# Optimization experiments

Hardware: AMD Instinct MI355X
Metric: run time of the kernel (lower is better)

## Reference

```python
import jax, jax.numpy as jnp
import numpy as np
from jax import lax

B, UD, YD, ZD, H, L, T = 256, 16, 16, 32, 128, 2, 2048


def _lin_params(key, out_dim, in_dim):
    k1, k2 = jax.random.split(key)
    s = 1.0 / np.sqrt(in_dim)
    w = jax.random.uniform(k1, (out_dim, in_dim), minval=-s, maxval=s, dtype=jnp.float32)
    b = jax.random.uniform(k2, (out_dim,), minval=-s, maxval=s, dtype=jnp.float32)
    return w, b


def setup_inputs() -> dict:
    key = jax.random.key(0)
    ks = iter(jax.random.split(key, 24))
    d = {}
    d["u"] = jax.random.normal(next(ks), (B, UD, T), dtype=jnp.float32)
    d["y"] = jax.random.normal(next(ks), (B, YD, T), dtype=jnp.float32)
    d["h0"] = jax.random.uniform(next(ks), (L, B, H), dtype=jnp.float32)  # torch.rand init
    d["phi_u_w1"], d["phi_u_b1"] = _lin_params(next(ks), H, UD)
    d["phi_u_w2"], d["phi_u_b2"] = _lin_params(next(ks), H, H)
    d["dynn_w1"], d["dynn_b1"] = _lin_params(next(ks), H, 2 * H)
    d["dynn_w2"], d["dynn_b2"] = _lin_params(next(ks), H, H)
    d["x_mean_w"], d["x_mean_b"] = _lin_params(next(ks), ZD, H)
    d["phi_x_w1"], d["phi_x_b1"] = _lin_params(next(ks), H, ZD)
    d["phi_x_w2"], d["phi_x_b2"] = _lin_params(next(ks), H, H)
    d["menn_w1"], d["menn_b1"] = _lin_params(next(ks), H, H)
    d["menn_w2"], d["menn_b2"] = _lin_params(next(ks), YD, H)
    s = 1.0 / np.sqrt(H)
    d["gru_wih"] = jax.random.uniform(next(ks), (L, 3 * H, H), minval=-s, maxval=s, dtype=jnp.float32)
    d["gru_whh"] = jax.random.uniform(next(ks), (L, 3 * H, H), minval=-s, maxval=s, dtype=jnp.float32)
    return d


def _mlp(x, w1, b1, w2, b2):
    # Linear -> ReLU -> Linear (torch Linear convention: x @ W.T + b)
    return jax.nn.relu(x @ w1.T + b1) @ w2.T + b2


def _gru_step(h, x_in, wih, whh):
    # h: (L, B, H); x_in: (B, H); nn.GRU with bias=False
    new_h = []
    inp = x_in
    for l in range(L):
        gi = inp @ wih[l].T           # (B, 3H)
        gh = h[l] @ whh[l].T          # (B, 3H)
        i_r, i_z, i_n = jnp.split(gi, 3, axis=-1)
        h_r, h_z, h_n = jnp.split(gh, 3, axis=-1)
        r = jax.nn.sigmoid(i_r + h_r)
        z = jax.nn.sigmoid(i_z + h_z)
        n = jnp.tanh(i_n + r * h_n)
        hl = (1.0 - z) * n + z * h[l]
        new_h.append(hl)
        inp = hl
    return jnp.stack(new_h)


def reference(u, y, h0, phi_u_w1, phi_u_b1, phi_u_w2, phi_u_b2,
              dynn_w1, dynn_b1, dynn_w2, dynn_b2, x_mean_w, x_mean_b,
              phi_x_w1, phi_x_b1, phi_x_w2, phi_x_b2,
              menn_w1, menn_b1, menn_w2, menn_b2, gru_wih, gru_whh):
    # mpnt_wt = -1 branch (0 >= mpnt_wt > -10): pure NN dynamics + measurement
    u_t = jnp.transpose(u, (2, 0, 1))  # (T, B, UD)
    y_t = jnp.transpose(y, (2, 0, 1))  # (T, B, YD)
    # phi_u has no recurrent dependency -> precompute over all timesteps
    pu = _mlp(u_t, phi_u_w1, phi_u_b1, phi_u_w2, phi_u_b2)  # (T, B, H)

    def step(h, inputs):
        pu_t, yt = inputs
        d = _mlp(jnp.concatenate([pu_t, h[-1]], axis=1), dynn_w1, dynn_b1, dynn_w2, dynn_b2)
        x_t = d @ x_mean_w.T + x_mean_b                 # (B, ZD)
        h_new = _gru_step(h, pu_t, gru_wih, gru_whh)
        px = _mlp(x_t, phi_x_w1, phi_x_b1, phi_x_w2, phi_x_b2)
        y_hat = _mlp(px, menn_w1, menn_b1, menn_w2, menn_b2)
        loss_t = jnp.sum((y_hat - yt) ** 2)
        return h_new, loss_t

    _, losses = lax.scan(step, h0, (pu, y_t))
    return jnp.sum(losses)
```

## Files before the change

### kernel.cpp

```cpp
#include <hip/hip_runtime.h>
#include <hip/hip_bf16.h>

#define TT 2048
#define BB 256
#define HH 128
#define UDIM 16
#define YDIM 16
#define ZDIM 32
#define H3 384

typedef __hip_bfloat16 bf16;
typedef _Float16 half2v __attribute__((ext_vector_type(2)));

constexpr int clog2(int x) { return x <= 1 ? 0 : 1 + clog2(x >> 1); }

template <int M_, int K_, int O_, bool RELU_>
__device__ __forceinline__ void rstage(const float* __restrict__ wfrag,
                                       const float* __restrict__ xin, int XS,
                                       float* __restrict__ ps,
                                       const float* __restrict__ bias,
                                       float* __restrict__ outb)
{
    constexpr int F = K_ / O_;
    const int T = threadIdx.x;
    const int jb = T & (M_ / 2 - 1);
    const int o  = T >> clog2(M_ / 2);
#pragma unroll
    for (int r = 0; r < 8; ++r) {
        float a0 = 0.f, a1 = 0.f;
#pragma unroll
        for (int g = 0; g < F; g += 4) {
            const float4 xv = *reinterpret_cast<const float4*>(&xin[r * XS + o * F + g]);
            a0 += xv.x * wfrag[g]     + xv.y * wfrag[g + 1]
                + xv.z * wfrag[g + 2] + xv.w * wfrag[g + 3];
            a1 += xv.x * wfrag[F + g]     + xv.y * wfrag[F + g + 1]
                + xv.z * wfrag[F + g + 2] + xv.w * wfrag[F + g + 3];
        }
        ps[r * 1024 + o * M_ + jb]           = a0;
        ps[r * 1024 + o * M_ + jb + M_ / 2]  = a1;
    }
    __syncthreads();
    for (int oi = T; oi < 8 * M_; oi += 512) {
        const int r = oi >> clog2(M_);
        const int j = oi & (M_ - 1);
        float s = bias[j];
#pragma unroll
        for (int o2 = 0; o2 < O_; ++o2) s += ps[r * 1024 + o2 * M_ + j];
        if (RELU_) s = fmaxf(s, 0.f);
        outb[r * M_ + j] = s;
    }
    __syncthreads();
}

template <int M_, int K_, int O_>
__device__ __forceinline__ void loadw(float* __restrict__ wfrag, const float* __restrict__ Wg)
{
    constexpr int F = K_ / O_;
    const int T = threadIdx.x;
    const int jb = T & (M_ / 2 - 1);
    const int o  = T >> clog2(M_ / 2);
#pragma unroll
    for (int h = 0; h < 2; ++h)
#pragma unroll
        for (int g = 0; g < F; g += 4)
            *reinterpret_cast<float4*>(&wfrag[h * F + g]) =
                *reinterpret_cast<const float4*>(&Wg[(jb + h * (M_ / 2)) * K_ + o * F + g]);
}

template <int M_, int K_, int O_>
__device__ __forceinline__ void loadw_h(half2v* __restrict__ wfrag, const float* __restrict__ Wg)
{
    constexpr int F = K_ / O_;
    const int T = threadIdx.x;
    const int jb = T & (M_ / 2 - 1);
    const int o  = T >> clog2(M_ / 2);
#pragma unroll
    for (int h = 0; h < 2; ++h)
#pragma unroll
        for (int g = 0; g < F / 2; ++g) {
            const float* s = &Wg[(jb + h * (M_ / 2)) * K_ + o * F + 2 * g];
            half2v v; v.x = (_Float16)s[0]; v.y = (_Float16)s[1];
            wfrag[h * (F / 2) + g] = v;
        }
}

template <int M_, int K_, int O_, bool RELU_>
__device__ __forceinline__ void rstage_h(const half2v* __restrict__ wfrag,
                                         const _Float16* __restrict__ xin, int XS,
                                         float* __restrict__ ps,
                                         const float* __restrict__ bias,
                                         _Float16* __restrict__ outb)
{
    constexpr int F = K_ / O_;
    constexpr int FH = F / 2;
    const int T = threadIdx.x;
    const int jb = T & (M_ / 2 - 1);
    const int o  = T >> clog2(M_ / 2);
#pragma unroll
    for (int r = 0; r < 8; ++r) {
        float a0 = 0.f, a1 = 0.f;
        const half2v* xv = reinterpret_cast<const half2v*>(xin + r * XS + o * F);
        if constexpr (FH >= 4) {
#pragma unroll
            for (int g4 = 0; g4 < FH / 4; ++g4) {
                half2v xt[4];
                *reinterpret_cast<float4*>(xt) = reinterpret_cast<const float4*>(xv)[g4];
#pragma unroll
                for (int e = 0; e < 4; ++e) {
                    a0 = __builtin_amdgcn_fdot2(xt[e], wfrag[g4 * 4 + e], a0, false);
                    a1 = __builtin_amdgcn_fdot2(xt[e], wfrag[FH + g4 * 4 + e], a1, false);
                }
            }
        } else {
            half2v xt[2];
            *reinterpret_cast<float2*>(xt) = *reinterpret_cast<const float2*>(xv);
            a0 = __builtin_amdgcn_fdot2(xt[0], wfrag[0], a0, false);
            a0 = __builtin_amdgcn_fdot2(xt[1], wfrag[1], a0, false);
            a1 = __builtin_amdgcn_fdot2(xt[0], wfrag[FH], a1, false);
            a1 = __builtin_amdgcn_fdot2(xt[1], wfrag[FH + 1], a1, false);
        }
        ps[r * 1024 + o * M_ + jb]           = a0;
        ps[r * 1024 + o * M_ + jb + M_ / 2]  = a1;
    }
    __syncthreads();
    for (int oi = T; oi < 8 * M_; oi += 512) {
        const int r = oi >> clog2(M_);
        const int j = oi & (M_ - 1);
        float s = bias[j];
#pragma unroll
        for (int o2 = 0; o2 < O_; ++o2) s += ps[r * 1024 + o2 * M_ + j];
        if (RELU_) s = fmaxf(s, 0.f);
        outb[r * M_ + j] = (_Float16)s;
    }
    __syncthreads();
}

__global__ __launch_bounds__(512, 2) void phi_u_kernel(
    const float* __restrict__ u, const float* __restrict__ w1, const float* __restrict__ b1,
    const float* __restrict__ w2, const float* __restrict__ b2,
    bf16* __restrict__ pu, int s0, int nrows)
{
    __shared__ __align__(16) float ps[8192];
    __shared__ __align__(16) float xc[8 * 16];
    __shared__ __align__(16) float bP[8 * 128];
    __shared__ __align__(16) float bias_l[256];
    const int T = threadIdx.x;
    if (T < 128) { bias_l[T] = b1[T]; bias_l[128 + T] = b2[T]; }
    const int jb = T & 63, o = T >> 6;
    float wa[4];
    wa[0] = w1[jb * 16 + o * 2];        wa[1] = w1[jb * 16 + o * 2 + 1];
    wa[2] = w1[(jb + 64) * 16 + o * 2]; wa[3] = w1[(jb + 64) * 16 + o * 2 + 1];
    float wb[32]; loadw<128, 128, 8>(wb, w2);
    __syncthreads();

    for (int tile = blockIdx.x; tile < nrows / 32; tile += gridDim.x) {
        const int n0 = tile * 32;
        const int b  = s0 + (n0 >> 11);
        const int t0 = n0 & (TT - 1);
#pragma unroll 1
        for (int rb = 0; rb < 4; ++rb) {
            if (T < 128) {
                const int r = T & 7, c = T >> 3;
                xc[r * 16 + c] = u[((size_t)b * UDIM + c) * TT + t0 + rb * 8 + r];
            }
            __syncthreads();
#pragma unroll
            for (int r = 0; r < 8; ++r) {
                const float x0 = xc[r * 16 + o * 2], x1 = xc[r * 16 + o * 2 + 1];
                ps[r * 1024 + o * 128 + jb]      = x0 * wa[0] + x1 * wa[1];
                ps[r * 1024 + o * 128 + jb + 64] = x0 * wa[2] + x1 * wa[3];
            }
            __syncthreads();
            for (int oi = T; oi < 8 * 128; oi += 512) {
                const int r = oi >> 7, j = oi & 127;
                float s = bias_l[j];
#pragma unroll
                for (int o2 = 0; o2 < 8; ++o2) s += ps[r * 1024 + o2 * 128 + j];
                bP[r * 128 + j] = fmaxf(s, 0.f);
            }
            __syncthreads();
            rstage<128, 128, 8, false>(wb, bP, 128, ps, bias_l + 128, bP);
            const int row0 = n0 + rb * 8;
            for (int oi = T; oi < 8 * 128; oi += 512) {
                const int r = oi >> 7, j = oi & 127;
                pu[(size_t)(row0 + r) * HH + j] = __float2bfloat16(bP[r * 128 + j]);
            }
            __syncthreads();
        }
    }
}

__device__ __forceinline__ void gmv(const half2v w[6][16], const _Float16* __restrict__ vb,
                                    int o, float* __restrict__ psL, int psb)
{
    const half2v* vec2 = reinterpret_cast<const half2v*>(vb) + o * 16;
    float a0 = 0.f, a1 = 0.f, a2 = 0.f, a3 = 0.f, a4 = 0.f, a5 = 0.f;
#pragma unroll
    for (int k4 = 0; k4 < 4; ++k4) {
        half2v xt[4];
        *reinterpret_cast<float4*>(xt) = reinterpret_cast<const float4*>(vec2)[k4];
#pragma unroll
        for (int e = 0; e < 4; ++e) {
            const int k = k4 * 4 + e;
            a0 = __builtin_amdgcn_fdot2(xt[e], w[0][k], a0, false);
            a1 = __builtin_amdgcn_fdot2(xt[e], w[1][k], a1, false);
            a2 = __builtin_amdgcn_fdot2(xt[e], w[2][k], a2, false);
            a3 = __builtin_amdgcn_fdot2(xt[e], w[3][k], a3, false);
            a4 = __builtin_amdgcn_fdot2(xt[e], w[4][k], a4, false);
            a5 = __builtin_amdgcn_fdot2(xt[e], w[5][k], a5, false);
        }
    }
    psL[psb]       = a0; psL[psb + 64]  = a1; psL[psb + 128] = a2;
    psL[psb + 192] = a3; psL[psb + 256] = a4; psL[psb + 320] = a5;
}

__global__ __launch_bounds__(512, 2) void gru_fused_kernel(
    const bf16* __restrict__ pu_in,
    const float* __restrict__ wih,
    const float* __restrict__ whh,
    const float* __restrict__ h0_g,
    bf16* __restrict__ hlast,
    int s0)
{
    const int t = threadIdx.x;
    __shared__ __align__(16) _Float16 x0h[HH];
    __shared__ __align__(16) _Float16 x1h[2][HH];
    __shared__ __align__(16) _Float16 h0h[HH];
    __shared__ __align__(16) _Float16 h1h[HH];
    __shared__ __align__(16) float ps[2 * 3072];

    const int g = t >> 6;
    const int m = g >> 2, o = g & 3;
    const int u = t & 63;
    const float* WbaseA = ((m == 0) ? wih : whh);
    const float* WbaseB = WbaseA + (size_t)H3 * HH;
    half2v wA[6][16], wB[6][16];
#pragma unroll
    for (int i = 0; i < 6; ++i) {
        const float* sA = &WbaseA[(u + 64 * i) * HH + o * 32];
        const float* sB = &WbaseB[(u + 64 * i) * HH + o * 32];
#pragma unroll
        for (int k = 0; k < 16; ++k) {
            half2v v; v.x = (_Float16)sA[2 * k]; v.y = (_Float16)sA[2 * k + 1];
            wA[i][k] = v;
            half2v w2; w2.x = (_Float16)sB[2 * k]; w2.y = (_Float16)sB[2 * k + 1];
            wB[i][k] = w2;
        }
    }
    float* psA = ps;
    float* psB = ps + 3072;
    const int psb = o * 768 + m * 384 + u;

    const bf16* xb = pu_in + (size_t)blockIdx.x * TT * HH;
    bf16* ob = hlast + (size_t)blockIdx.x * TT * HH;

    float hreg = 0.f;
    if (t < HH) {
        hreg = h0_g[(size_t)(s0 + blockIdx.x) * HH + t];
        h0h[t] = (_Float16)hreg;
        x0h[t] = (_Float16)__bfloat162float(xb[t]);
    } else if (t < 2 * HH) {
        const int j = t - HH;
        hreg = h0_g[((size_t)BB + s0 + blockIdx.x) * HH + j];
        h1h[j] = (_Float16)hreg;
    }
    __syncthreads();

#pragma unroll 1
    for (int i = 0; i <= TT; ++i) {
        float xnext = 0.f;
        if (t < HH && i + 1 < TT)
            xnext = __bfloat162float(xb[(size_t)(i + 1) * HH + t]);
        if (i < TT)  gmv(wA, (m == 0) ? x0h : h0h, o, psA, psb);
        if (i >= 1)  gmv(wB, (m == 0) ? x1h[(i + 1) & 1] : h1h, o, psB, psb);
        __syncthreads();
        if (t < HH) {
            if (i < TT) {
                const int j = t;
                float gir = 0.f, giz = 0.f, gin = 0.f, ghr = 0.f, ghz = 0.f, ghn = 0.f;
#pragma unroll
                for (int o2 = 0; o2 < 4; ++o2) {
                    const float* pp = psA + o2 * 768;
                    gir += pp[j];        giz += pp[128 + j]; gin += pp[256 + j];
                    ghr += pp[384 + j];  ghz += pp[512 + j]; ghn += pp[640 + j];
                }
                const float rg = 1.f / (1.f + __expf(-(gir + ghr)));
                const float zg = 1.f / (1.f + __expf(-(giz + ghz)));
                const float narg = gin + rg * ghn;
                const float e2 = __expf(2.f * fabsf(narg));
                float ng = 1.f - 2.f / (e2 + 1.f);
                ng = (narg < 0.f) ? -ng : ng;
                const float hn = (1.f - zg) * ng + zg * hreg;
                h0h[j] = (_Float16)hn;
                x1h[i & 1][j] = (_Float16)hn;
                x0h[j] = (_Float16)xnext;
                hreg = hn;
            }
        } else if (t < 2 * HH) {
            if (i >= 1) {
                const int j = t - HH;
                float gir = 0.f, giz = 0.f, gin = 0.f, ghr = 0.f, ghz = 0.f, ghn = 0.f;
#pragma unroll
                for (int o2 = 0; o2 < 4; ++o2) {
                    const float* pp = psB + o2 * 768;
                    gir += pp[j];        giz += pp[128 + j]; gin += pp[256 + j];
                    ghr += pp[384 + j];  ghz += pp[512 + j]; ghn += pp[640 + j];
                }
                const float rg = 1.f / (1.f + __expf(-(gir + ghr)));
                const float zg = 1.f / (1.f + __expf(-(giz + ghz)));
                const float narg = gin + rg * ghn;
                const float e2 = __expf(2.f * fabsf(narg));
                float ng = 1.f - 2.f / (e2 + 1.f);
                ng = (narg < 0.f) ? -ng : ng;
                ob[(size_t)(i - 1) * HH + j] = __float2bfloat16(hreg);
                const float hn = (1.f - zg) * ng + zg * hreg;
                h1h[j] = (_Float16)hn;
                hreg = hn;
            }
        }
        __syncthreads();
    }
}

__device__ __forceinline__ void stage_xc_h(_Float16* __restrict__ xc,
                                           const bf16* __restrict__ pu,
                                           const bf16* __restrict__ hl,
                                           int n0, int rb)
{
    const int T = threadIdx.x;
    const int base = n0 + rb * 8;
#pragma unroll
    for (int i = 0; i < 4; ++i) {
        const int idx = T + i * 512;
        const int r = idx >> 8, k = idx & 255;
        const size_t row = (size_t)(base + r);
        xc[r * 256 + k] = (_Float16)((k < 128) ? __bfloat162float(pu[row * HH + k])
                                               : __bfloat162float(hl[row * HH + (k - 128)]));
    }
}

__global__ __launch_bounds__(512, 4) void head_kernel(
    const bf16* __restrict__ pu, const bf16* __restrict__ hlast, const float* __restrict__ y_g,
    const float* __restrict__ dw1, const float* __restrict__ db1,
    const float* __restrict__ dw2, const float* __restrict__ db2,
    const float* __restrict__ xw, const float* __restrict__ xb,
    const float* __restrict__ pxw1, const float* __restrict__ pxb1,
    const float* __restrict__ pxw2, const float* __restrict__ pxb2,
    const float* __restrict__ mw1, const float* __restrict__ mb1,
    const float* __restrict__ mw2, const float* __restrict__ mb2,
    float* __restrict__ out, int s0, int nrows)
{
    __shared__ __align__(16) float ps[8192];
    __shared__ __align__(16) _Float16 xc[8 * 256];
    __shared__ __align__(16) _Float16 bP[8 * 128];
    __shared__ __align__(16) _Float16 bQ[8 * 128];
    __shared__ __align__(16) float bias_l[528];
    __shared__ float red[8];
    const int T = threadIdx.x;

    if (T < 128) bias_l[T]       = db1[T];
    if (T < 128) bias_l[256 + T] = pxb2[T];
    if (T < 128) bias_l[384 + T] = mb1[T];
    if (T < 16)  bias_l[512 + T] = mb2[T];

    for (int idx = T; idx < 4096; idx += 512) {
        const int z = idx >> 7, k = idx & 127;
        float s = 0.f;
        for (int m2 = 0; m2 < 128; ++m2) s += xw[z * 128 + m2] * dw2[m2 * 128 + k];
        ps[idx] = s;
    }
    if (T < 32) {
        float c = xb[T];
        for (int m2 = 0; m2 < 128; ++m2) c += xw[T * 128 + m2] * db2[m2];
        ps[4096 + T] = c;
    }
    __syncthreads();
    half2v wc[16];
    {
        const int jbw = T & 63, ow = T >> 6;
#pragma unroll
        for (int h = 0; h < 2; ++h) {
            const int j = jbw + h * 64;
#pragma unroll
            for (int gg = 0; gg < 8; ++gg) {
                const int k0 = ow * 16 + 2 * gg;
                float s0 = 0.f, s1 = 0.f;
#pragma unroll
                for (int z = 0; z < 32; ++z) {
                    const float p = pxw1[j * 32 + z];
                    s0 += p * ps[z * 128 + k0];
                    s1 += p * ps[z * 128 + k0 + 1];
                }
                half2v v; v.x = (_Float16)s0; v.y = (_Float16)s1;
                wc[h * 8 + gg] = v;
            }
        }
    }
    if (T < 128) {
        float s = pxb1[T];
#pragma unroll
        for (int z = 0; z < 32; ++z) s += pxw1[T * 32 + z] * ps[4096 + z];
        bias_l[128 + T] = s;
    }

    half2v w1[32]; loadw_h<128, 256, 8 >(w1, dw1);
    half2v w5[16]; loadw_h<128, 128, 8 >(w5, pxw2);
    half2v w6[16]; loadw_h<128, 128, 8 >(w6, mw1);
    const int jb7 = T & 7, o7 = T >> 3;
    half2v w7a, w7b;
    w7a.x = (_Float16)mw2[jb7 * 128 + 2 * o7];
    w7a.y = (_Float16)mw2[jb7 * 128 + 2 * o7 + 1];
    w7b.x = (_Float16)mw2[(jb7 + 8) * 128 + 2 * o7];
    w7b.y = (_Float16)mw2[(jb7 + 8) * 128 + 2 * o7 + 1];

    float lossreg = 0.f;

    for (int tile = blockIdx.x; tile < nrows / 32; tile += gridDim.x) {
        const int n0 = tile * 32;
        const int b  = s0 + (n0 >> 11);
        const int t0 = n0 & (TT - 1);
        stage_xc_h(xc, pu, hlast, n0, 0);
#pragma unroll 1
        for (int rb = 0; rb < 4; ++rb) {
            __syncthreads();
            rstage_h<128, 256, 8, true >(w1, xc, 256, ps, bias_l + 0,   bP);
            rstage_h<128, 128, 8, true >(wc, bP, 128, ps, bias_l + 128, bQ);
            rstage_h<128, 128, 8, false>(w5, bQ, 128, ps, bias_l + 256, bP);
            rstage_h<128, 128, 8, true >(w6, bP, 128, ps, bias_l + 384, bQ);
#pragma unroll
            for (int r = 0; r < 8; ++r) {
                const half2v xv = *reinterpret_cast<const half2v*>(&bQ[r * 128 + 2 * o7]);
                ps[r * 1024 + o7 * 16 + jb7]     = __builtin_amdgcn_fdot2(xv, w7a, 0.f, false);
                ps[r * 1024 + o7 * 16 + jb7 + 8] = __builtin_amdgcn_fdot2(xv, w7b, 0.f, false);
            }
            if (rb < 3) stage_xc_h(xc, pu, hlast, n0, rb + 1);
            __syncthreads();
            if (T < 128) {
                const int r = T >> 4, j = T & 15;
                float s = bias_l[512 + j];
#pragma unroll
                for (int o2 = 0; o2 < 64; ++o2) s += ps[r * 1024 + o2 * 16 + j];
                const int trow = t0 + rb * 8 + r;
                const float yv = y_g[((size_t)b * YDIM + j) * TT + trow];
                const float d = s - yv;
                lossreg += d * d;
            }
        }
    }
    __syncthreads();
#pragma unroll
    for (int off = 32; off > 0; off >>= 1) lossreg += __shfl_down(lossreg, off, 64);
    if ((T & 63) == 0) red[T >> 6] = lossreg;
    __syncthreads();
    if (T == 0) {
        float s = 0.f;
#pragma unroll
        for (int i = 0; i < 8; ++i) s += red[i];
        atomicAdd(out, s);
    }
}

__global__ void zero_out_kernel(float* o) { o[0] = 0.f; }

extern "C" void kernel_launch(void* const* d_in, const int* in_sizes, int n_in,
                              void* d_out, int out_size, void* d_ws, size_t ws_size,
                              hipStream_t stream)
{
    (void)in_sizes; (void)n_in; (void)out_size;
    const float* u    = (const float*)d_in[0];
    const float* y    = (const float*)d_in[1];
    const float* h0   = (const float*)d_in[2];
    const float* puw1 = (const float*)d_in[3];
    const float* pub1 = (const float*)d_in[4];
    const float* puw2 = (const float*)d_in[5];
    const float* pub2 = (const float*)d_in[6];
    const float* dw1  = (const float*)d_in[7];
    const float* db1  = (const float*)d_in[8];
    const float* dw2  = (const float*)d_in[9];
    const float* db2  = (const float*)d_in[10];
    const float* xw   = (const float*)d_in[11];
    const float* xbi  = (const float*)d_in[12];
    const float* pxw1 = (const float*)d_in[13];
    const float* pxb1 = (const float*)d_in[14];
    const float* pxw2 = (const float*)d_in[15];
    const float* pxb2 = (const float*)d_in[16];
    const float* mw1  = (const float*)d_in[17];
    const float* mb1  = (const float*)d_in[18];
    const float* mw2  = (const float*)d_in[19];
    const float* mb2  = (const float*)d_in[20];
    const float* gwih = (const float*)d_in[21];
    const float* gwhh = (const float*)d_in[22];

    const size_t per_sample = (size_t)TT * HH * 2 * 2;
    int C = BB;
    while (C > 1 && (size_t)C * per_sample > ws_size) C >>= 1;
    bf16* puB = (bf16*)d_ws;
    bf16* hlB = puB + (size_t)C * TT * HH;

    zero_out_kernel<<<1, 1, 0, stream>>>((float*)d_out);
    for (int s0 = 0; s0 < BB; s0 += C) {
        phi_u_kernel<<<512, 512, 0, stream>>>(u, puw1, pub1, puw2, pub2, puB, s0, C * TT);
        gru_fused_kernel<<<C, 512, 0, stream>>>(puB, gwih, gwhh, h0, hlB, s0);
        head_kernel<<<512, 512, 0, stream>>>(puB, hlB, y,
                                             dw1, db1, dw2, db2, xw, xbi,
                                             pxw1, pxb1, pxw2, pxb2,
                                             mw1, mb1, mw2, mb2,
                                             (float*)d_out, s0, C * TT);
    }
}
```

Baseline: 4.839 ms.

## Batch 16 sequences per block in GRU recurrence using MFMA f16 matmuls

Replaces the per-sequence GRU kernel, which used fdot2 matrix-vector products with one block per batch element, with an MFMA kernel where each block processes 16 sequences together. GRU weights for both layers are held in registers as f16 B-fragments, and hidden and input states sit in swizzled LDS tiles to avoid bank conflicts. The two layers now run in sequence within each timestep instead of being skewed across steps. The grid shrinks to C/16 blocks, so fewer CUs are used, and register pressure from 48 weight fragments is high.

```diff
diff --git a/kernel.cpp b/kernel.cpp
--- a/kernel.cpp
+++ b/kernel.cpp
@@ -8,11 +8,19 @@
 #define YDIM 16
 #define ZDIM 32
 #define H3 384
+#define GG 16
 
 typedef __hip_bfloat16 bf16;
 typedef _Float16 half2v __attribute__((ext_vector_type(2)));
+typedef _Float16 f16x8 __attribute__((ext_vector_type(8)));
+typedef float f32x4 __attribute__((ext_vector_type(4)));
+typedef unsigned short us4 __attribute__((ext_vector_type(4)));
 
 constexpr int clog2(int x) { return x <= 1 ? 0 : 1 + clog2(x >> 1); }
+
+__device__ __forceinline__ float bf2f(unsigned short b) {
+    return __uint_as_float((unsigned int)b << 16);
+}
 
 template <int M_, int K_, int O_, bool RELU_>
 __device__ __forceinline__ void rstage(const float* __restrict__ wfrag,
@@ -190,31 +198,11 @@
     }
 }
 
-__device__ __forceinline__ void gmv(const half2v w[6][16], const _Float16* __restrict__ vb,
-                                    int o, float* __restrict__ psL, int psb)
-{
-    const half2v* vec2 = reinterpret_cast<const half2v*>(vb) + o * 16;
-    float a0 = 0.f, a1 = 0.f, a2 = 0.f, a3 = 0.f, a4 = 0.f, a5 = 0.f;
-#pragma unroll
-    for (int k4 = 0; k4 < 4; ++k4) {
-        half2v xt[4];
-        *reinterpret_cast<float4*>(xt) = reinterpret_cast<const float4*>(vec2)[k4];
-#pragma unroll
-        for (int e = 0; e < 4; ++e) {
-            const int k = k4 * 4 + e;
-            a0 = __builtin_amdgcn_fdot2(xt[e], w[0][k], a0, false);
-            a1 = __builtin_amdgcn_fdot2(xt[e], w[1][k], a1, false);
-            a2 = __builtin_amdgcn_fdot2(xt[e], w[2][k], a2, false);
-            a3 = __builtin_amdgcn_fdot2(xt[e], w[3][k], a3, false);
-            a4 = __builtin_amdgcn_fdot2(xt[e], w[4][k], a4, false);
-            a5 = __builtin_amdgcn_fdot2(xt[e], w[5][k], a5, false);
-        }
-    }
-    psL[psb]       = a0; psL[psb + 64]  = a1; psL[psb + 128] = a2;
-    psL[psb + 192] = a3; psL[psb + 256] = a4; psL[psb + 320] = a5;
-}
-
-__global__ __launch_bounds__(512, 2) void gru_fused_kernel(
+__device__ __forceinline__ int swzi(int s, int j) {
+    return s * 128 + ((((j >> 3) ^ (s & 7)) << 3) | (j & 7));
+}
+
+__global__ __launch_bounds__(512, 2) void gru_mfma_kernel(
     const bf16* __restrict__ pu_in,
     const float* __restrict__ wih,
     const float* __restrict__ whh,
@@ -222,103 +210,140 @@
     bf16* __restrict__ hlast,
     int s0)
 {
-    const int t = threadIdx.x;
-    __shared__ __align__(16) _Float16 x0h[HH];
-    __shared__ __align__(16) _Float16 x1h[2][HH];
-    __shared__ __align__(16) _Float16 h0h[HH];
-    __shared__ __align__(16) _Float16 h1h[HH];
-    __shared__ __align__(16) float ps[2 * 3072];
-
-    const int g = t >> 6;
-    const int m = g >> 2, o = g & 3;
-    const int u = t & 63;
-    const float* WbaseA = ((m == 0) ? wih : whh);
-    const float* WbaseB = WbaseA + (size_t)H3 * HH;
-    half2v wA[6][16], wB[6][16];
-#pragma unroll
-    for (int i = 0; i < 6; ++i) {
-        const float* sA = &WbaseA[(u + 64 * i) * HH + o * 32];
-        const float* sB = &WbaseB[(u + 64 * i) * HH + o * 32];
-#pragma unroll
-        for (int k = 0; k < 16; ++k) {
-            half2v v; v.x = (_Float16)sA[2 * k]; v.y = (_Float16)sA[2 * k + 1];
-            wA[i][k] = v;
-            half2v w2; w2.x = (_Float16)sB[2 * k]; w2.y = (_Float16)sB[2 * k + 1];
-            wB[i][k] = w2;
-        }
-    }
-    float* psA = ps;
-    float* psB = ps + 3072;
-    const int psb = o * 768 + m * 384 + u;
-
-    const bf16* xb = pu_in + (size_t)blockIdx.x * TT * HH;
-    bf16* ob = hlast + (size_t)blockIdx.x * TT * HH;
-
-    float hreg = 0.f;
-    if (t < HH) {
-        hreg = h0_g[(size_t)(s0 + blockIdx.x) * HH + t];
-        h0h[t] = (_Float16)hreg;
-        x0h[t] = (_Float16)__bfloat162float(xb[t]);
-    } else if (t < 2 * HH) {
-        const int j = t - HH;
-        hreg = h0_g[((size_t)BB + s0 + blockIdx.x) * HH + j];
-        h1h[j] = (_Float16)hreg;
-    }
-    __syncthreads();
-
+    const int T = threadIdx.x;
+    const int w = T >> 6, l = T & 63;
+    const int lj = l & 15, lk = l >> 4;
+    __shared__ __align__(16) _Float16 Xl[2][GG * 128];
+    __shared__ __align__(16) _Float16 H0l[GG * 128];
+    __shared__ __align__(16) _Float16 H1l[GG * 128];
+
+    f16x8 wB[48];
+#pragma unroll
+    for (int L = 0; L < 2; ++L)
+#pragma unroll
+        for (int tt = 0; tt < 3; ++tt)
+#pragma unroll
+            for (int m = 0; m < 2; ++m) {
+                const float* Wm = (m == 0 ? wih : whh) + (size_t)L * H3 * HH
+                                  + (size_t)((w + 8 * tt) * 16 + lj) * HH;
+#pragma unroll
+                for (int kk = 0; kk < 4; ++kk) {
+                    const float* src = Wm + kk * 32 + lk * 8;
+                    f16x8 v;
+#pragma unroll
+                    for (int e = 0; e < 8; ++e) v[e] = (_Float16)src[e];
+                    wB[((L * 3 + tt) * 2 + m) * 4 + kk] = v;
+                }
+            }
+
+    const int blk = blockIdx.x;
+    const bf16* xg = pu_in + (size_t)blk * GG * TT * HH;
+    bf16* ob = hlast + (size_t)blk * GG * TT * HH;
+
+    float hp0[4], hp1[4];
+#pragma unroll
+    for (int r = 0; r < 4; ++r) {
+        const int s = lk * 4 + r, j = 16 * w + lj;
+        hp0[r] = h0_g[(size_t)(s0 + blk * GG + s) * HH + j];
+        hp1[r] = h0_g[((size_t)BB + s0 + blk * GG + s) * HH + j];
+    }
+#pragma unroll
+    for (int q = 0; q < 8; ++q) {
+        const int idx = T + q * 512;
+        const int s = (idx >> 7) & 15, j = idx & 127;
+        const float v = h0_g[((size_t)(idx >> 11) * BB + s0 + blk * GG + s) * HH + j];
+        ((idx >> 11) ? H1l : H0l)[swzi(s, j)] = (_Float16)v;
+    }
+    {
+        const int sx = T >> 5, jx = (T * 4) & 127;
+        const us4 xp = *reinterpret_cast<const us4*>(&xg[(size_t)sx * TT * HH + jx]);
+        _Float16 xc4[4];
+#pragma unroll
+        for (int e = 0; e < 4; ++e) {
+            const unsigned short usv = xp[e];
+            xc4[e] = (_Float16)bf2f(usv);
+        }
+        *reinterpret_cast<float2*>(&Xl[0][swzi(sx, jx)]) = *reinterpret_cast<float2*>(xc4);
+    }
+    __syncthreads();
+
+    const int jown = 16 * w + lj;
+    int cur = 0;
 #pragma unroll 1
-    for (int i = 0; i <= TT; ++i) {
-        float xnext = 0.f;
-        if (t < HH && i + 1 < TT)
-            xnext = __bfloat162float(xb[(size_t)(i + 1) * HH + t]);
-        if (i < TT)  gmv(wA, (m == 0) ? x0h : h0h, o, psA, psb);
-        if (i >= 1)  gmv(wB, (m == 0) ? x1h[(i + 1) & 1] : h1h, o, psB, psb);
+    for (int i = 0; i < TT; ++i) {
+        const int sx = T >> 5, jx = (T * 4) & 127;
+        us4 xpre = {0, 0, 0, 0};
+        if (i + 1 < TT)
+            xpre = *reinterpret_cast<const us4*>(&xg[((size_t)sx * TT + i + 1) * HH + jx]);
+
+        f32x4 aR = {0,0,0,0}, aZ = {0,0,0,0}, aNi = {0,0,0,0}, aNh = {0,0,0,0};
+#pragma unroll
+        for (int kk = 0; kk < 4; ++kk) {
+            const int aoff = lj * 128 + (((kk * 4 + lk) ^ (lj & 7)) << 3);
+            const f16x8 ax = *reinterpret_cast<const f16x8*>(&Xl[cur][aoff]);
+            const f16x8 ah = *reinterpret_cast<const f16x8*>(&H0l[aoff]);
+            aR  = __builtin_amdgcn_mfma_f32_16x16x32_f16(ax, wB[0  + kk], aR, 0, 0, 0);
+            aR  = __builtin_amdgcn_mfma_f32_16x16x32_f16(ah, wB[4  + kk], aR, 0, 0, 0);
+            aZ  = __builtin_amdgcn_mfma_f32_16x16x32_f16(ax, wB[8  + kk], aZ, 0, 0, 0);
+            aZ  = __builtin_amdgcn_mfma_f32_16x16x32_f16(ah, wB[12 + kk], aZ, 0, 0, 0);
+            aNi = __builtin_amdgcn_mfma_f32_16x16x32_f16(ax, wB[16 + kk], aNi, 0, 0, 0);
+            aNh = __builtin_amdgcn_mfma_f32_16x16x32_f16(ah, wB[20 + kk], aNh, 0, 0, 0);
+        }
         __syncthreads();
-        if (t < HH) {
-            if (i < TT) {
-                const int j = t;
-                float gir = 0.f, giz = 0.f, gin = 0.f, ghr = 0.f, ghz = 0.f, ghn = 0.f;
-#pragma unroll
-                for (int o2 = 0; o2 < 4; ++o2) {
-                    const float* pp = psA + o2 * 768;
-                    gir += pp[j];        giz += pp[128 + j]; gin += pp[256 + j];
-                    ghr += pp[384 + j];  ghz += pp[512 + j]; ghn += pp[640 + j];
-                }
-                const float rg = 1.f / (1.f + __expf(-(gir + ghr)));
-                const float zg = 1.f / (1.f + __expf(-(giz + ghz)));
-                const float narg = gin + rg * ghn;
-                const float e2 = __expf(2.f * fabsf(narg));
-                float ng = 1.f - 2.f / (e2 + 1.f);
-                ng = (narg < 0.f) ? -ng : ng;
-                const float hn = (1.f - zg) * ng + zg * hreg;
-                h0h[j] = (_Float16)hn;
-                x1h[i & 1][j] = (_Float16)hn;
-                x0h[j] = (_Float16)xnext;
-                hreg = hn;
-            }
-        } else if (t < 2 * HH) {
-            if (i >= 1) {
-                const int j = t - HH;
-                float gir = 0.f, giz = 0.f, gin = 0.f, ghr = 0.f, ghz = 0.f, ghn = 0.f;
-#pragma unroll
-                for (int o2 = 0; o2 < 4; ++o2) {
-                    const float* pp = psB + o2 * 768;
-                    gir += pp[j];        giz += pp[128 + j]; gin += pp[256 + j];
-                    ghr += pp[384 + j];  ghz += pp[512 + j]; ghn += pp[640 + j];
-                }
-                const float rg = 1.f / (1.f + __expf(-(gir + ghr)));
-                const float zg = 1.f / (1.f + __expf(-(giz + ghz)));
-                const float narg = gin + rg * ghn;
-                const float e2 = __expf(2.f * fabsf(narg));
-                float ng = 1.f - 2.f / (e2 + 1.f);
-                ng = (narg < 0.f) ? -ng : ng;
-                ob[(size_t)(i - 1) * HH + j] = __float2bfloat16(hreg);
-                const float hn = (1.f - zg) * ng + zg * hreg;
-                h1h[j] = (_Float16)hn;
-                hreg = hn;
-            }
+#pragma unroll
+        for (int r = 0; r < 4; ++r) {
+            const int s = lk * 4 + r;
+            const float rg = 1.f / (1.f + __expf(-aR[r]));
+            const float zg = 1.f / (1.f + __expf(-aZ[r]));
+            const float narg = aNi[r] + rg * aNh[r];
+            const float e2 = __expf(2.f * fabsf(narg));
+            float ng = 1.f - 2.f / (e2 + 1.f);
+            ng = (narg < 0.f) ? -ng : ng;
+            const float hn = (1.f - zg) * ng + zg * hp0[r];
+            hp0[r] = hn;
+            H0l[swzi(s, jown)] = (_Float16)hn;
+        }
+        if (i + 1 < TT) {
+            _Float16 xc4[4];
+#pragma unroll
+            for (int e = 0; e < 4; ++e) {
+                const unsigned short usv = xpre[e];
+                xc4[e] = (_Float16)bf2f(usv);
+            }
+            *reinterpret_cast<float2*>(&Xl[cur ^ 1][swzi(sx, jx)]) =
+                *reinterpret_cast<float2*>(xc4);
         }
         __syncthreads();
+
+        f32x4 bR = {0,0,0,0}, bZ = {0,0,0,0}, bNi = {0,0,0,0}, bNh = {0,0,0,0};
+#pragma unroll
+        for (int kk = 0; kk < 4; ++kk) {
+            const int aoff = lj * 128 + (((kk * 4 + lk) ^ (lj & 7)) << 3);
+            const f16x8 ax = *reinterpret_cast<const f16x8*>(&H0l[aoff]);
+            const f16x8 ah = *reinterpret_cast<const f16x8*>(&H1l[aoff]);
+            bR  = __builtin_amdgcn_mfma_f32_16x16x32_f16(ax, wB[24 + kk], bR, 0, 0, 0);
+            bR  = __builtin_amdgcn_mfma_f32_16x16x32_f16(ah, wB[28 + kk], bR, 0, 0, 0);
+            bZ  = __builtin_amdgcn_mfma_f32_16x16x32_f16(ax, wB[32 + kk], bZ, 0, 0, 0);
+            bZ  = __builtin_amdgcn_mfma_f32_16x16x32_f16(ah, wB[36 + kk], bZ, 0, 0, 0);
+            bNi = __builtin_amdgcn_mfma_f32_16x16x32_f16(ax, wB[40 + kk], bNi, 0, 0, 0);
+            bNh = __builtin_amdgcn_mfma_f32_16x16x32_f16(ah, wB[44 + kk], bNh, 0, 0, 0);
+        }
+        __syncthreads();
+#pragma unroll
+        for (int r = 0; r < 4; ++r) {
+            const int s = lk * 4 + r;
+            ob[((size_t)s * TT + i) * HH + jown] = __float2bfloat16(hp1[r]);
+            const float rg = 1.f / (1.f + __expf(-bR[r]));
+            const float zg = 1.f / (1.f + __expf(-bZ[r]));
+            const float narg = bNi[r] + rg * bNh[r];
+            const float e2 = __expf(2.f * fabsf(narg));
+            float ng = 1.f - 2.f / (e2 + 1.f);
+            ng = (narg < 0.f) ? -ng : ng;
+            const float hn = (1.f - zg) * ng + zg * hp1[r];
+            hp1[r] = hn;
+            H1l[swzi(s, jown)] = (_Float16)hn;
+        }
+        cur ^= 1;
     }
 }
 
@@ -384,14 +409,14 @@
 #pragma unroll
             for (int gg = 0; gg < 8; ++gg) {
                 const int k0 = ow * 16 + 2 * gg;
-                float s0 = 0.f, s1 = 0.f;
+                float s0_ = 0.f, s1_ = 0.f;
 #pragma unroll
                 for (int z = 0; z < 32; ++z) {
                     const float p = pxw1[j * 32 + z];
-                    s0 += p * ps[z * 128 + k0];
-                    s1 += p * ps[z * 128 + k0 + 1];
+                    s0_ += p * ps[z * 128 + k0];
+                    s1_ += p * ps[z * 128 + k0 + 1];
                 }
-                half2v v; v.x = (_Float16)s0; v.y = (_Float16)s1;
+                half2v v; v.x = (_Float16)s0_; v.y = (_Float16)s1_;
                 wc[h * 8 + gg] = v;
             }
         }
@@ -493,14 +518,14 @@
 
     const size_t per_sample = (size_t)TT * HH * 2 * 2;
     int C = BB;
-    while (C > 1 && (size_t)C * per_sample > ws_size) C >>= 1;
+    while (C > GG && (size_t)C * per_sample > ws_size) C >>= 1;
     bf16* puB = (bf16*)d_ws;
     bf16* hlB = puB + (size_t)C * TT * HH;
 
     zero_out_kernel<<<1, 1, 0, stream>>>((float*)d_out);
     for (int s0 = 0; s0 < BB; s0 += C) {
         phi_u_kernel<<<512, 512, 0, stream>>>(u, puw1, pub1, puw2, pub2, puB, s0, C * TT);
-        gru_fused_kernel<<<C, 512, 0, stream>>>(puB, gwih, gwhh, h0, hlB, s0);
+        gru_mfma_kernel<<<C / GG, 512, 0, stream>>>(puB, gwih, gwhh, h0, hlB, s0);
         head_kernel<<<512, 512, 0, stream>>>(puB, hlB, y,
                                              dw1, db1, dw2, db2, xw, xbi,
                                              pxw1, pxb1, pxw2, pxb2,
```

Measured after the change: 8.745 ms. 80.7% more time.
